# Kernel tuning notes

Hardware: AMD Instinct MI355X
Metric: run time of the kernel (lower is better)

The kernel has to match this reference:

```python
import jax, jax.numpy as jnp
import numpy as np

N, E, IN_DIM, OUT_DIM, HEADS = 50000, 800000, 128, 64, 2
NEG_SLOPE = 0.2  # DGL GATConv default leaky_relu slope


def setup_inputs() -> dict:
    key = jax.random.key(0)
    ks = jax.random.split(key, 11)
    p = lambda k, shape: jax.random.normal(k, shape, jnp.float32) * 0.05
    return dict(
        feature=jax.random.normal(ks[0], (N, IN_DIM), jnp.float32),
        src=jax.random.randint(ks[1], (E,), 0, N, jnp.int32),
        dst=jax.random.randint(ks[2], (E,), 0, N, jnp.int32),
        W1=p(ks[3], (IN_DIM, HEADS * OUT_DIM)),
        al1=p(ks[4], (HEADS, OUT_DIM)),
        ar1=p(ks[5], (HEADS, OUT_DIM)),
        b1=p(ks[6], (HEADS * OUT_DIM,)),
        W2=p(ks[7], (HEADS * OUT_DIM, OUT_DIM)),
        al2=p(ks[8], (1, OUT_DIM)),
        ar2=p(ks[9], (1, OUT_DIM)),
        b2=p(ks[10], (OUT_DIM,)),
    )


def gat_conv(x, W, al, ar, b, src, dst, n_nodes):
    # DGL GATConv (eval mode): fc -> per-node attn halves -> edge leaky_relu
    # -> edge-softmax grouped by dst -> scatter-weighted sum -> + bias
    H, D = al.shape
    h = (x @ W).reshape(n_nodes, H, D)               # [N,H,D]
    el = jnp.einsum('nhd,hd->nh', h, al)             # [N,H]
    er = jnp.einsum('nhd,hd->nh', h, ar)             # [N,H]
    e = jax.nn.leaky_relu(el[src] + er[dst], NEG_SLOPE)  # [E,H]
    m = jax.ops.segment_max(e, dst, num_segments=n_nodes)
    m = jnp.where(jnp.isfinite(m), m, 0.0)           # guard isolated dst nodes
    ex = jnp.exp(e - m[dst])                         # [E,H]
    s = jax.ops.segment_sum(ex, dst, num_segments=n_nodes)
    alpha = ex / s[dst]                              # edge-softmax weights
    out = jax.ops.segment_sum(alpha[:, :, None] * h[src], dst,
                              num_segments=n_nodes)  # [N,H,D]
    return out + b.reshape(H, D)


def reference(feature, src, dst, W1, al1, ar1, b1, W2, al2, ar2, b2):
    h1 = jax.nn.elu(gat_conv(feature, W1, al1, ar1, b1, src, dst, N))  # [N,2,D]
    h2 = gat_conv(h1.reshape(N, -1), W2, al2, ar2, b2, src, dst, N)    # [N,1,D]
    return (h1.mean(axis=1) + h2[:, 0, :]) * 0.5
```

## Files before the change

### kernel.cpp

```cpp
#include <hip/hip_runtime.h>
#include <hip/hip_fp16.h>
#include <math.h>

#define NNODES 50000
#define NEDGES 800000
#define CSR_STRIDE 48
#define NBUCKET 256
#define CHUNK 196
#define BCAP 4096
#define EPB 4096

typedef short bf16x8 __attribute__((ext_vector_type(8)));
typedef float f32x4  __attribute__((ext_vector_type(4)));

__device__ __forceinline__ unsigned bfpack(float a, float b) {
    unsigned ua = __float_as_uint(a), ub = __float_as_uint(b);
    ua = (ua + 0x7fffu + ((ua >> 16) & 1u)) >> 16;
    ub = (ub + 0x7fffu + ((ub >> 16) & 1u)) >> 16;
    return ua | (ub << 16);
}
__device__ __forceinline__ unsigned h2pack(float a, float b) {
    __half2 h = __floats2half2_rn(a, b);
    return *(unsigned*)&h;
}
__device__ __forceinline__ float hlo(unsigned u) {
    union { unsigned u; __half2 h; } c; c.u = u; return __half2float(c.h.x);
}
__device__ __forceinline__ float hhi(unsigned u) {
    union { unsigned u; __half2 h; } c; c.u = u; return __half2float(c.h.y);
}

__global__ __launch_bounds__(256) void bucketA_kernel(
    const int* __restrict__ src, const int* __restrict__ dst,
    int* __restrict__ bcnt, unsigned* __restrict__ bbuf) {
    __shared__ int lcnt[NBUCKET];
    __shared__ int lcur[NBUCKET];
    const int tid = threadIdx.x;
    lcnt[tid] = 0;
    __syncthreads();
    const int e0 = blockIdx.x * EPB;
    int e1 = e0 + EPB; if (e1 > NEDGES) e1 = NEDGES;
    for (int e = e0 + tid; e < e1; e += 256)
        atomicAdd(&lcnt[dst[e] / CHUNK], 1);
    __syncthreads();
    int c = lcnt[tid];
    int base = 0;
    if (c > 0) base = atomicAdd(&bcnt[tid], c);
    lcur[tid] = tid * BCAP + base;
    __syncthreads();
    for (int e = e0 + tid; e < e1; e += 256) {
        int d = dst[e], s = src[e];
        int b = d / CHUNK;
        int pos = atomicAdd(&lcur[b], 1);
        if (pos < (b + 1) * BCAP)
            bbuf[pos] = ((unsigned)(d - b * CHUNK) << 16) | (unsigned)s;
    }
}

__global__ __launch_bounds__(256) void bucketB_kernel(
    const int* __restrict__ bcnt, const unsigned* __restrict__ bbuf,
    int* __restrict__ deg, unsigned short* __restrict__ pcsr) {
    const int b = blockIdx.x, tid = threadIdx.x;
    const int n0 = b * CHUNK;
    int ncnt = NNODES - n0; if (ncnt > CHUNK) ncnt = CHUNK;
    __shared__ int ldeg[CHUNK];
    __shared__ unsigned short lcsr[CHUNK * CSR_STRIDE];
    for (int i = tid; i < CHUNK; i += 256) ldeg[i] = 0;
    __syncthreads();
    int cnt = bcnt[b]; if (cnt > BCAP) cnt = BCAP;
    const unsigned* bb = bbuf + (size_t)b * BCAP;
    for (int i = tid; i < cnt; i += 256) {
        unsigned e = bb[i];
        int ln = e >> 16;
        int p = atomicAdd(&ldeg[ln], 1);
        if (p < CSR_STRIDE) lcsr[ln * CSR_STRIDE + p] = (unsigned short)(e & 0xffffu);
    }
    __syncthreads();
    for (int i = tid; i < ncnt; i += 256) deg[n0 + i] = ldeg[i];
    const int nv = ncnt * (CSR_STRIDE / 8);
    uint4* d4 = (uint4*)(pcsr + (size_t)n0 * CSR_STRIDE);
    const uint4* s4 = (const uint4*)lcsr;
    for (int i = tid; i < nv; i += 256) d4[i] = s4[i];
}

__global__ __launch_bounds__(256) void wt_kernel(const float* __restrict__ W1,
                                                 const float* __restrict__ W2,
                                                 unsigned* __restrict__ W1t,
                                                 unsigned* __restrict__ W2t,
                                                 int* __restrict__ bcnt) {
    if (blockIdx.x == 0) bcnt[threadIdx.x] = 0;
    int w = blockIdx.x * 256 + threadIdx.x;
    if (w < 8192) {
        int n = w >> 6, j = w & 63;
        W1t[w] = bfpack(W1[(2 * j) * 128 + n], W1[(2 * j + 1) * 128 + n]);
    } else {
        int w2 = w - 8192;
        int n = w2 >> 6, j = w2 & 63;
        W2t[w2] = bfpack(W2[(2 * j) * 64 + n], W2[(2 * j + 1) * 64 + n]);
    }
}

__global__ __launch_bounds__(256) void gemm1_kernel(
    const float* __restrict__ feat, const unsigned* __restrict__ Wt,
    const float* __restrict__ al, const float* __restrict__ ar,
    unsigned* __restrict__ h, float* __restrict__ el, float* __restrict__ er) {
    __shared__ unsigned Wb[128 * 68];
    __shared__ unsigned Ab[64 * 68];
    const int tid = threadIdx.x;
    const int n0  = blockIdx.x * 64;

#pragma unroll
    for (int i = 0; i < 8; ++i) {
        int id = i * 256 + tid;
        int n = id >> 4, c = (id & 15) * 4;
        *(uint4*)&Wb[n * 68 + c] = *(const uint4*)&Wt[n * 64 + c];
    }
#pragma unroll
    for (int i = 0; i < 8; ++i) {
        int f = i * 256 + tid;
        int m = f >> 5, cf = (f & 31) * 4;
        float4 v = make_float4(0.f, 0.f, 0.f, 0.f);
        if (n0 + m < NNODES)
            v = *(const float4*)&feat[(size_t)(n0 + m) * 128 + cf];
        uint2 p = {bfpack(v.x, v.y), bfpack(v.z, v.w)};
        *(uint2*)&Ab[m * 68 + cf / 2] = p;
    }
    __syncthreads();

    const int w  = tid >> 6;
    const int l  = tid & 63;
    const int ml = l & 15;
    const int q  = l >> 4;
    f32x4 acc[8];
#pragma unroll
    for (int t = 0; t < 8; ++t) acc[t] = (f32x4){0.f, 0.f, 0.f, 0.f};

#pragma unroll
    for (int kc = 0; kc < 4; ++kc) {
        const int kw = kc * 16 + q * 4;
        uint4 a4 = *(uint4*)&Ab[(16 * w + ml) * 68 + kw];
        bf16x8 af = *(bf16x8*)&a4;
#pragma unroll
        for (int t = 0; t < 8; ++t) {
            uint4 b4 = *(uint4*)&Wb[(t * 16 + ml) * 68 + kw];
            bf16x8 bf = *(bf16x8*)&b4;
            acc[t] = __builtin_amdgcn_mfma_f32_16x16x32_bf16(af, bf, acc[t], 0, 0, 0);
        }
    }

    float av[8], rv[8];
#pragma unroll
    for (int t = 0; t < 8; ++t) { av[t] = al[t * 16 + ml]; rv[t] = ar[t * 16 + ml]; }

#pragma unroll
    for (int r = 0; r < 4; ++r) {
        const int node = n0 + 16 * w + q * 4 + r;
        float e0 = 0.f, e1 = 0.f, f0 = 0.f, f1 = 0.f;
#pragma unroll
        for (int t = 0; t < 8; ++t) {
            float v = acc[t][r];
            if (t < 4) { e0 = fmaf(v, av[t], e0); f0 = fmaf(v, rv[t], f0); }
            else       { e1 = fmaf(v, av[t], e1); f1 = fmaf(v, rv[t], f1); }
            float pv = __shfl_xor(v, 1);
            if ((ml & 1) == 0 && node < NNODES)
                h[(size_t)node * 64 + t * 8 + (ml >> 1)] = h2pack(v, pv);
        }
#pragma unroll
        for (int mm = 1; mm <= 8; mm <<= 1) {
            e0 += __shfl_xor(e0, mm); e1 += __shfl_xor(e1, mm);
            f0 += __shfl_xor(f0, mm); f1 += __shfl_xor(f1, mm);
        }
        if (ml == 0 && node < NNODES) {
            el[node * 2 + 0] = e0; el[node * 2 + 1] = e1;
            er[node * 2 + 0] = f0; er[node * 2 + 1] = f1;
        }
    }
}

__global__ __launch_bounds__(256) void gemm2_kernel(
    const unsigned* __restrict__ h1b, const unsigned* __restrict__ Wt,
    const float* __restrict__ al, const float* __restrict__ ar,
    unsigned* __restrict__ h2, float* __restrict__ el, float* __restrict__ er) {
    __shared__ unsigned Wb[64 * 68];
    __shared__ unsigned Ab[64 * 68];
    const int tid = threadIdx.x;
    const int n0  = blockIdx.x * 64;

#pragma unroll
    for (int i = 0; i < 4; ++i) {
        int id = i * 256 + tid;
        int n = id >> 4, c = (id & 15) * 4;
        *(uint4*)&Wb[n * 68 + c] = *(const uint4*)&Wt[n * 64 + c];
    }
#pragma unroll
    for (int i = 0; i < 4; ++i) {
        int id = i * 256 + tid;
        int m = id >> 4, c = (id & 15) * 4;
        uint4 v = make_uint4(0u, 0u, 0u, 0u);
        if (n0 + m < NNODES)
            v = *(const uint4*)&h1b[(size_t)(n0 + m) * 64 + c];
        *(uint4*)&Ab[m * 68 + c] = v;
    }
    __syncthreads();

    const int w  = tid >> 6;
    const int l  = tid & 63;
    const int ml = l & 15;
    const int q  = l >> 4;
    f32x4 acc[4];
#pragma unroll
    for (int t = 0; t < 4; ++t) acc[t] = (f32x4){0.f, 0.f, 0.f, 0.f};

#pragma unroll
    for (int kc = 0; kc < 4; ++kc) {
        const int kw = kc * 16 + q * 4;
        uint4 a4 = *(uint4*)&Ab[(16 * w + ml) * 68 + kw];
        bf16x8 af = *(bf16x8*)&a4;
#pragma unroll
        for (int t = 0; t < 4; ++t) {
            uint4 b4 = *(uint4*)&Wb[(t * 16 + ml) * 68 + kw];
            bf16x8 bf = *(bf16x8*)&b4;
            acc[t] = __builtin_amdgcn_mfma_f32_16x16x32_bf16(af, bf, acc[t], 0, 0, 0);
        }
    }

    float av[4], rv[4];
#pragma unroll
    for (int t = 0; t < 4; ++t) { av[t] = al[t * 16 + ml]; rv[t] = ar[t * 16 + ml]; }

#pragma unroll
    for (int r = 0; r < 4; ++r) {
        const int node = n0 + 16 * w + q * 4 + r;
        float e0 = 0.f, f0 = 0.f;
#pragma unroll
        for (int t = 0; t < 4; ++t) {
            float v = acc[t][r];
            e0 = fmaf(v, av[t], e0);
            f0 = fmaf(v, rv[t], f0);
            float pv = __shfl_xor(v, 1);
            if ((ml & 1) == 0 && node < NNODES)
                h2[(size_t)node * 32 + t * 8 + (ml >> 1)] = h2pack(v, pv);
        }
#pragma unroll
        for (int mm = 1; mm <= 8; mm <<= 1) {
            e0 += __shfl_xor(e0, mm);
            f0 += __shfl_xor(f0, mm);
        }
        if (ml == 0 && node < NNODES) { el[node] = e0; er[node] = f0; }
    }
}

#define FMA8(hv, A)                                              \
    a0r = fmaf(hlo(hv.x), A, a0r); a1r = fmaf(hhi(hv.x), A, a1r); \
    a2r = fmaf(hlo(hv.y), A, a2r); a3r = fmaf(hhi(hv.y), A, a3r); \
    a4r = fmaf(hlo(hv.z), A, a4r); a5r = fmaf(hhi(hv.z), A, a5r); \
    a6r = fmaf(hlo(hv.w), A, a6r); a7r = fmaf(hhi(hv.w), A, a7r);

__global__ __launch_bounds__(256) void aggregate1_kernel(
    const int* __restrict__ degv,
    const unsigned short* __restrict__ csr_src,
    const float* __restrict__ el, const float* __restrict__ er,
    const unsigned* __restrict__ hh, const float* __restrict__ bias,
    unsigned* __restrict__ h1b, float* __restrict__ hm) {
    const int wid  = (blockIdx.x * 256 + threadIdx.x) >> 6;
    const int lane = threadIdx.x & 63;
    const int g    = lane >> 4;
    const int l16  = lane & 15;
    const int gb   = g * 16;
    const int node = wid * 4 + g;
    if (node >= NNODES) return;
    const int row = node * CSR_STRIDE;
    int deg = degv[node];
    deg = deg < CSR_STRIDE ? deg : CSR_STRIDE;
    const float er0 = er[node * 2 + 0];
    const float er1 = er[node * 2 + 1];
    const bool hsel = (l16 >= 8);
    const unsigned* __restrict__ hq = hh + 4 * l16;

    int s0 = 0;
    if (l16 < deg) s0 = (int)csr_src[row + l16];

    uint4 hv[16];
#pragma unroll
    for (int j = 0; j < 16; ++j) {
        int s = __shfl(s0, gb + j);
        hv[j] = *(const uint4*)(hq + (size_t)s * 64);
    }

    float2 e2 = *(const float2*)&el[s0 * 2];
    float a = e2.x + er0; a = a > 0.f ? a : 0.2f * a;
    float b = e2.y + er1; b = b > 0.f ? b : 0.2f * b;
    float v0 = (l16 < deg) ? a : -1e30f;
    float v1 = (l16 < deg) ? b : -1e30f;
    float m0 = v0, m1 = v1;
    int   s1 = 0, s2 = 0;
    float va1 = -1e30f, vb1 = -1e30f, va2 = -1e30f, vb2 = -1e30f;
    if (deg > 16) {
        if (16 + l16 < deg) {
            s1 = (int)csr_src[row + 16 + l16];
            float2 ee = *(const float2*)&el[s1 * 2];
            float aa = ee.x + er0; va1 = aa > 0.f ? aa : 0.2f * aa;
            float bb = ee.y + er1; vb1 = bb > 0.f ? bb : 0.2f * bb;
            m0 = fmaxf(m0, va1); m1 = fmaxf(m1, vb1);
        }
        if (32 + l16 < deg) {
            s2 = (int)csr_src[row + 32 + l16];
            float2 ee = *(const float2*)&el[s2 * 2];
            float aa = ee.x + er0; va2 = aa > 0.f ? aa : 0.2f * aa;
            float bb = ee.y + er1; vb2 = bb > 0.f ? bb : 0.2f * bb;
            m0 = fmaxf(m0, va2); m1 = fmaxf(m1, vb2);
        }
    }
#pragma unroll
    for (int off = 8; off > 0; off >>= 1) {
        m0 = fmaxf(m0, __shfl_xor(m0, off));
        m1 = fmaxf(m1, __shfl_xor(m1, off));
    }
    float p0 = __expf(v0 - m0),  p1 = __expf(v1 - m1);
    float q0 = __expf(va1 - m0), q1 = __expf(vb1 - m1);
    float r0 = __expf(va2 - m0), r1 = __expf(vb2 - m1);
    float ssum0 = p0 + q0 + r0, ssum1 = p1 + q1 + r1;
#pragma unroll
    for (int off = 8; off > 0; off >>= 1) {
        ssum0 += __shfl_xor(ssum0, off);
        ssum1 += __shfl_xor(ssum1, off);
    }

    float a0r = 0.f, a1r = 0.f, a2r = 0.f, a3r = 0.f;
    float a4r = 0.f, a5r = 0.f, a6r = 0.f, a7r = 0.f;
#pragma unroll
    for (int j = 0; j < 16; ++j) {
        float x = __shfl(p0, gb + j);
        float y = __shfl(p1, gb + j);
        float A = hsel ? y : x;
        FMA8(hv[j], A)
    }
    if (deg > 16) {
        uint4 hw[16];
#pragma unroll
        for (int j = 0; j < 16; ++j) {
            int s = __shfl(s1, gb + j);
            hw[j] = *(const uint4*)(hq + (size_t)s * 64);
        }
#pragma unroll
        for (int j = 0; j < 16; ++j) {
            float x = __shfl(q0, gb + j);
            float y = __shfl(q1, gb + j);
            float A = hsel ? y : x;
            FMA8(hw[j], A)
        }
    }
    if (deg > 32) {
        uint4 hz[16];
#pragma unroll
        for (int j = 0; j < 16; ++j) {
            int s = __shfl(s2, gb + j);
            hz[j] = *(const uint4*)(hq + (size_t)s * 64);
        }
#pragma unroll
        for (int j = 0; j < 16; ++j) {
            float x = __shfl(r0, gb + j);
            float y = __shfl(r1, gb + j);
            float A = hsel ? y : x;
            FMA8(hz[j], A)
        }
    }

    const float ssum = hsel ? ssum1 : ssum0;
    const float inv  = (deg > 0) ? 1.f / ssum : 0.f;
    float4 b0 = *(const float4*)&bias[8 * l16];
    float4 b1 = *(const float4*)&bias[8 * l16 + 4];
    float o0 = fmaf(a0r, inv, b0.x), o1 = fmaf(a1r, inv, b0.y);
    float o2 = fmaf(a2r, inv, b0.z), o3 = fmaf(a3r, inv, b0.w);
    float o4 = fmaf(a4r, inv, b1.x), o5 = fmaf(a5r, inv, b1.y);
    float o6 = fmaf(a6r, inv, b1.z), o7 = fmaf(a7r, inv, b1.w);
    o0 = o0 > 0.f ? o0 : (__expf(o0) - 1.f);
    o1 = o1 > 0.f ? o1 : (__expf(o1) - 1.f);
    o2 = o2 > 0.f ? o2 : (__expf(o2) - 1.f);
    o3 = o3 > 0.f ? o3 : (__expf(o3) - 1.f);
    o4 = o4 > 0.f ? o4 : (__expf(o4) - 1.f);
    o5 = o5 > 0.f ? o5 : (__expf(o5) - 1.f);
    o6 = o6 > 0.f ? o6 : (__expf(o6) - 1.f);
    o7 = o7 > 0.f ? o7 : (__expf(o7) - 1.f);

    uint4 pk;
    pk.x = bfpack(o0, o1); pk.y = bfpack(o2, o3);
    pk.z = bfpack(o4, o5); pk.w = bfpack(o6, o7);
    *(uint4*)&h1b[(size_t)node * 64 + 4 * l16] = pk;

    float n0_ = 0.5f * (o0 + __shfl_xor(o0, 8));
    float n1_ = 0.5f * (o1 + __shfl_xor(o1, 8));
    float n2_ = 0.5f * (o2 + __shfl_xor(o2, 8));
    float n3_ = 0.5f * (o3 + __shfl_xor(o3, 8));
    float n4_ = 0.5f * (o4 + __shfl_xor(o4, 8));
    float n5_ = 0.5f * (o5 + __shfl_xor(o5, 8));
    float n6_ = 0.5f * (o6 + __shfl_xor(o6, 8));
    float n7_ = 0.5f * (o7 + __shfl_xor(o7, 8));
    if (l16 < 8) {
        *(float4*)&hm[(size_t)node * 64 + 8 * l16]     = make_float4(n0_, n1_, n2_, n3_);
        *(float4*)&hm[(size_t)node * 64 + 8 * l16 + 4] = make_float4(n4_, n5_, n6_, n7_);
    }
}

#define FMA4(hv, P)                                            \
    ax = fmaf(hlo(hv.x), P, ax); ay = fmaf(hhi(hv.x), P, ay);  \
    az = fmaf(hlo(hv.y), P, az); aw = fmaf(hhi(hv.y), P, aw);

__global__ __launch_bounds__(256) void aggregate2_kernel(
    const int* __restrict__ degv,
    const unsigned short* __restrict__ csr_src,
    const float* __restrict__ el, const float* __restrict__ er,
    const unsigned* __restrict__ hh, const float* __restrict__ bias,
    const float* __restrict__ hm, float* __restrict__ outp) {
    const int wid  = (blockIdx.x * 256 + threadIdx.x) >> 6;
    const int lane = threadIdx.x & 63;
    const int g    = lane >> 4;
    const int l16  = lane & 15;
    const int gb   = g * 16;
    const int node = wid * 4 + g;
    if (node >= NNODES) return;
    const int row = node * CSR_STRIDE;
    int deg = degv[node];
    deg = deg < CSR_STRIDE ? deg : CSR_STRIDE;
    const float erd = er[node];
    const unsigned* __restrict__ hq = hh + 2 * l16;

    int s0 = 0;
    if (l16 < deg) s0 = (int)csr_src[row + l16];

    uint2 hv[16];
#pragma unroll
    for (int j = 0; j < 16; ++j) {
        int s = __shfl(s0, gb + j);
        hv[j] = *(const uint2*)(hq + (size_t)s * 32);
    }

    float v = el[s0] + erd;
    v = v > 0.f ? v : 0.2f * v;
    float v0 = (l16 < deg) ? v : -1e30f;
    float m = v0;
    int   s1 = 0, s2 = 0;
    float va1 = -1e30f, va2 = -1e30f;
    if (deg > 16) {
        if (16 + l16 < deg) {
            s1 = (int)csr_src[row + 16 + l16];
            float vv = el[s1] + erd;
            va1 = vv > 0.f ? vv : 0.2f * vv;
            m = fmaxf(m, va1);
        }
        if (32 + l16 < deg) {
            s2 = (int)csr_src[row + 32 + l16];
            float vv = el[s2] + erd;
            va2 = vv > 0.f ? vv : 0.2f * vv;
            m = fmaxf(m, va2);
        }
    }
#pragma unroll
    for (int off = 8; off > 0; off >>= 1) m = fmaxf(m, __shfl_xor(m, off));
    float p0 = __expf(v0 - m);
    float q0 = __expf(va1 - m);
    float r0 = __expf(va2 - m);
    float ssum = p0 + q0 + r0;
#pragma unroll
    for (int off = 8; off > 0; off >>= 1) ssum += __shfl_xor(ssum, off);

    float ax = 0.f, ay = 0.f, az = 0.f, aw = 0.f;
#pragma unroll
    for (int j = 0; j < 16; ++j) {
        float p = __shfl(p0, gb + j);
        FMA4(hv[j], p)
    }
    if (deg > 16) {
        uint2 hw[16];
#pragma unroll
        for (int j = 0; j < 16; ++j) {
            int s = __shfl(s1, gb + j);
            hw[j] = *(const uint2*)(hq + (size_t)s * 32);
        }
#pragma unroll
        for (int j = 0; j < 16; ++j) {
            float p = __shfl(q0, gb + j);
            FMA4(hw[j], p)
        }
    }
    if (deg > 32) {
        uint2 hz[16];
#pragma unroll
        for (int j = 0; j < 16; ++j) {
            int s = __shfl(s2, gb + j);
            hz[j] = *(const uint2*)(hq + (size_t)s * 32);
        }
#pragma unroll
        for (int j = 0; j < 16; ++j) {
            float p = __shfl(r0, gb + j);
            FMA4(hz[j], p)
        }
    }

    float inv = (deg > 0) ? 1.f / ssum : 0.f;
    float4 hmv = *(const float4*)&hm[(size_t)node * 64 + 4 * l16];
    float4 bb  = *(const float4*)&bias[4 * l16];
    float o0 = (hmv.x + fmaf(ax, inv, bb.x)) * 0.5f;
    float o1 = (hmv.y + fmaf(ay, inv, bb.y)) * 0.5f;
    float o2 = (hmv.z + fmaf(az, inv, bb.z)) * 0.5f;
    float o3 = (hmv.w + fmaf(aw, inv, bb.w)) * 0.5f;
    *(float4*)&outp[(size_t)node * 64 + 4 * l16] = make_float4(o0, o1, o2, o3);
}


extern "C" void kernel_launch(void* const* d_in, const int* in_sizes, int n_in,
                              void* d_out, int out_size, void* d_ws, size_t ws_size,
                              hipStream_t stream) {
    const float* feat = (const float*)d_in[0];
    const int*   src  = (const int*)d_in[1];
    const int*   dst  = (const int*)d_in[2];
    const float* W1   = (const float*)d_in[3];
    const float* al1  = (const float*)d_in[4];
    const float* ar1  = (const float*)d_in[5];
    const float* b1   = (const float*)d_in[6];
    const float* W2   = (const float*)d_in[7];
    const float* al2  = (const float*)d_in[8];
    const float* ar2  = (const float*)d_in[9];
    const float* b2   = (const float*)d_in[10];
    float* out = (float*)d_out;

    int*            bcnt   = (int*)d_ws;
    int*            ideg   = bcnt + NBUCKET;
    unsigned*       iw1t   = (unsigned*)(ideg + NNODES);
    unsigned*       iw2t   = iw1t + 8192;
    unsigned short* pcsr   = (unsigned short*)(iw2t + 4096);
    unsigned*       gH1    = (unsigned*)(pcsr + (size_t)NNODES * CSR_STRIDE);
    unsigned*       bbuf   = gH1;
    unsigned*       gH2    = gH1;
    unsigned*       h1b    = gH1 + (size_t)NNODES * 64;
    float*          hmean  = (float*)(h1b + (size_t)NNODES * 64);
    float*          fEl1   = hmean + (size_t)NNODES * 64;
    float*          fEr1   = fEl1 + (size_t)NNODES * 2;
    float*          fEl2   = fEr1 + (size_t)NNODES * 2;
    float*          fEr2   = fEl2 + (size_t)NNODES;

    wt_kernel<<<48, 256, 0, stream>>>(W1, W2, iw1t, iw2t, bcnt);
    bucketA_kernel<<<(NEDGES + EPB - 1) / EPB, 256, 0, stream>>>(src, dst, bcnt, bbuf);
    bucketB_kernel<<<NBUCKET, 256, 0, stream>>>(bcnt, bbuf, ideg, pcsr);

    gemm1_kernel<<<(NNODES + 63) / 64, 256, 0, stream>>>(feat, iw1t, al1, ar1,
                                                         gH1, fEl1, fEr1);
    aggregate1_kernel<<<(NNODES + 15) / 16, 256, 0, stream>>>(
        ideg, pcsr, fEl1, fEr1, gH1, b1, h1b, hmean);

    gemm2_kernel<<<(NNODES + 63) / 64, 256, 0, stream>>>(h1b, iw2t, al2, ar2,
                                                         gH2, fEl2, fEr2);
    aggregate2_kernel<<<(NNODES + 15) / 16, 256, 0, stream>>>(
        ideg, pcsr, fEl2, fEr2, gH2, b2, hmean, out);
}
```

Baseline: 207.9 us.

## Merge independent prep stages into shared launches to cut kernel count

Folds weight transposition into the edge-bucketing kernel as extra blocks, and runs CSR build blocks inside the gemm1 launch since the two are independent. The bucket counter is now zeroed with a memset. The bucket buffer moves to the h1b region so it no longer aliases gH1, which gemm1 writes while CSR build blocks are still reading buckets. This removes launch gaps and lets independent work overlap, at the cost of branchy kernels with shared LDS sizing.

```diff
diff --git a/kernel.cpp b/kernel.cpp
--- a/kernel.cpp
+++ b/kernel.cpp
@@ -9,6 +9,8 @@
 #define CHUNK 196
 #define BCAP 4096
 #define EPB 4096
+#define NBLK_A ((NEDGES + EPB - 1) / EPB)
+#define NBLK_G1 ((NNODES + 63) / 64)
 
 typedef short bf16x8 __attribute__((ext_vector_type(8)));
 typedef float f32x4  __attribute__((ext_vector_type(4)));
@@ -30,84 +32,84 @@
     union { unsigned u; __half2 h; } c; c.u = u; return __half2float(c.h.y);
 }
 
-__global__ __launch_bounds__(256) void bucketA_kernel(
+__global__ __launch_bounds__(256) void prep_kernel(
     const int* __restrict__ src, const int* __restrict__ dst,
-    int* __restrict__ bcnt, unsigned* __restrict__ bbuf) {
-    __shared__ int lcnt[NBUCKET];
-    __shared__ int lcur[NBUCKET];
+    int* __restrict__ bcnt, unsigned* __restrict__ bbuf,
+    const float* __restrict__ W1, const float* __restrict__ W2,
+    unsigned* __restrict__ W1t, unsigned* __restrict__ W2t) {
     const int tid = threadIdx.x;
-    lcnt[tid] = 0;
-    __syncthreads();
-    const int e0 = blockIdx.x * EPB;
-    int e1 = e0 + EPB; if (e1 > NEDGES) e1 = NEDGES;
-    for (int e = e0 + tid; e < e1; e += 256)
-        atomicAdd(&lcnt[dst[e] / CHUNK], 1);
-    __syncthreads();
-    int c = lcnt[tid];
-    int base = 0;
-    if (c > 0) base = atomicAdd(&bcnt[tid], c);
-    lcur[tid] = tid * BCAP + base;
-    __syncthreads();
-    for (int e = e0 + tid; e < e1; e += 256) {
-        int d = dst[e], s = src[e];
-        int b = d / CHUNK;
-        int pos = atomicAdd(&lcur[b], 1);
-        if (pos < (b + 1) * BCAP)
-            bbuf[pos] = ((unsigned)(d - b * CHUNK) << 16) | (unsigned)s;
-    }
-}
-
-__global__ __launch_bounds__(256) void bucketB_kernel(
+    if (blockIdx.x < NBLK_A) {
+        __shared__ int lcnt[NBUCKET];
+        __shared__ int lcur[NBUCKET];
+        lcnt[tid] = 0;
+        __syncthreads();
+        const int e0 = blockIdx.x * EPB;
+        int e1 = e0 + EPB; if (e1 > NEDGES) e1 = NEDGES;
+        for (int e = e0 + tid; e < e1; e += 256)
+            atomicAdd(&lcnt[dst[e] / CHUNK], 1);
+        __syncthreads();
+        int c = lcnt[tid];
+        int base = 0;
+        if (c > 0) base = atomicAdd(&bcnt[tid], c);
+        lcur[tid] = tid * BCAP + base;
+        __syncthreads();
+        for (int e = e0 + tid; e < e1; e += 256) {
+            int d = dst[e], s = src[e];
+            int b = d / CHUNK;
+            int pos = atomicAdd(&lcur[b], 1);
+            if (pos < (b + 1) * BCAP)
+                bbuf[pos] = ((unsigned)(d - b * CHUNK) << 16) | (unsigned)s;
+        }
+    } else {
+        int w = (blockIdx.x - NBLK_A) * 256 + tid;
+        if (w < 8192) {
+            int n = w >> 6, j = w & 63;
+            W1t[w] = bfpack(W1[(2 * j) * 128 + n], W1[(2 * j + 1) * 128 + n]);
+        } else {
+            int w2 = w - 8192;
+            int n = w2 >> 6, j = w2 & 63;
+            W2t[w2] = bfpack(W2[(2 * j) * 64 + n], W2[(2 * j + 1) * 64 + n]);
+        }
+    }
+}
+
+__global__ __launch_bounds__(256) void build_gemm1_kernel(
     const int* __restrict__ bcnt, const unsigned* __restrict__ bbuf,
-    int* __restrict__ deg, unsigned short* __restrict__ pcsr) {
-    const int b = blockIdx.x, tid = threadIdx.x;
-    const int n0 = b * CHUNK;
-    int ncnt = NNODES - n0; if (ncnt > CHUNK) ncnt = CHUNK;
-    __shared__ int ldeg[CHUNK];
-    __shared__ unsigned short lcsr[CHUNK * CSR_STRIDE];
-    for (int i = tid; i < CHUNK; i += 256) ldeg[i] = 0;
-    __syncthreads();
-    int cnt = bcnt[b]; if (cnt > BCAP) cnt = BCAP;
-    const unsigned* bb = bbuf + (size_t)b * BCAP;
-    for (int i = tid; i < cnt; i += 256) {
-        unsigned e = bb[i];
-        int ln = e >> 16;
-        int p = atomicAdd(&ldeg[ln], 1);
-        if (p < CSR_STRIDE) lcsr[ln * CSR_STRIDE + p] = (unsigned short)(e & 0xffffu);
-    }
-    __syncthreads();
-    for (int i = tid; i < ncnt; i += 256) deg[n0 + i] = ldeg[i];
-    const int nv = ncnt * (CSR_STRIDE / 8);
-    uint4* d4 = (uint4*)(pcsr + (size_t)n0 * CSR_STRIDE);
-    const uint4* s4 = (const uint4*)lcsr;
-    for (int i = tid; i < nv; i += 256) d4[i] = s4[i];
-}
-
-__global__ __launch_bounds__(256) void wt_kernel(const float* __restrict__ W1,
-                                                 const float* __restrict__ W2,
-                                                 unsigned* __restrict__ W1t,
-                                                 unsigned* __restrict__ W2t,
-                                                 int* __restrict__ bcnt) {
-    if (blockIdx.x == 0) bcnt[threadIdx.x] = 0;
-    int w = blockIdx.x * 256 + threadIdx.x;
-    if (w < 8192) {
-        int n = w >> 6, j = w & 63;
-        W1t[w] = bfpack(W1[(2 * j) * 128 + n], W1[(2 * j + 1) * 128 + n]);
-    } else {
-        int w2 = w - 8192;
-        int n = w2 >> 6, j = w2 & 63;
-        W2t[w2] = bfpack(W2[(2 * j) * 64 + n], W2[(2 * j + 1) * 64 + n]);
-    }
-}
-
-__global__ __launch_bounds__(256) void gemm1_kernel(
+    int* __restrict__ deg, unsigned short* __restrict__ pcsr,
     const float* __restrict__ feat, const unsigned* __restrict__ Wt,
     const float* __restrict__ al, const float* __restrict__ ar,
     unsigned* __restrict__ h, float* __restrict__ el, float* __restrict__ er) {
-    __shared__ unsigned Wb[128 * 68];
-    __shared__ unsigned Ab[64 * 68];
+    __shared__ uint4 smem4[(128 * 68 + 64 * 68) / 4];
     const int tid = threadIdx.x;
-    const int n0  = blockIdx.x * 64;
+
+    if (blockIdx.x < NBUCKET) {
+        int* ldeg = (int*)smem4;
+        unsigned short* lcsr = (unsigned short*)(ldeg + CHUNK);
+        const int b = blockIdx.x;
+        const int n0 = b * CHUNK;
+        int ncnt = NNODES - n0; if (ncnt > CHUNK) ncnt = CHUNK;
+        for (int i = tid; i < CHUNK; i += 256) ldeg[i] = 0;
+        __syncthreads();
+        int cnt = bcnt[b]; if (cnt > BCAP) cnt = BCAP;
+        const unsigned* bb = bbuf + (size_t)b * BCAP;
+        for (int i = tid; i < cnt; i += 256) {
+            unsigned e = bb[i];
+            int ln = e >> 16;
+            int p = atomicAdd(&ldeg[ln], 1);
+            if (p < CSR_STRIDE) lcsr[ln * CSR_STRIDE + p] = (unsigned short)(e & 0xffffu);
+        }
+        __syncthreads();
+        for (int i = tid; i < ncnt; i += 256) deg[n0 + i] = ldeg[i];
+        const int nv = ncnt * (CSR_STRIDE / 8);
+        uint4* d4 = (uint4*)(pcsr + (size_t)n0 * CSR_STRIDE);
+        const uint4* s4 = (const uint4*)lcsr;
+        for (int i = tid; i < nv; i += 256) d4[i] = s4[i];
+        return;
+    }
+
+    unsigned* Wb = (unsigned*)smem4;
+    unsigned* Ab = Wb + 128 * 68;
+    const int n0 = (blockIdx.x - NBUCKET) * 64;
 
 #pragma unroll
     for (int i = 0; i < 8; ++i) {
@@ -530,26 +532,24 @@
     unsigned*       iw2t   = iw1t + 8192;
     unsigned short* pcsr   = (unsigned short*)(iw2t + 4096);
     unsigned*       gH1    = (unsigned*)(pcsr + (size_t)NNODES * CSR_STRIDE);
-    unsigned*       bbuf   = gH1;
     unsigned*       gH2    = gH1;
     unsigned*       h1b    = gH1 + (size_t)NNODES * 64;
+    unsigned*       bbuf   = h1b;
     float*          hmean  = (float*)(h1b + (size_t)NNODES * 64);
     float*          fEl1   = hmean + (size_t)NNODES * 64;
     float*          fEr1   = fEl1 + (size_t)NNODES * 2;
     float*          fEl2   = fEr1 + (size_t)NNODES * 2;
     float*          fEr2   = fEl2 + (size_t)NNODES;
 
-    wt_kernel<<<48, 256, 0, stream>>>(W1, W2, iw1t, iw2t, bcnt);
-    bucketA_kernel<<<(NEDGES + EPB - 1) / EPB, 256, 0, stream>>>(src, dst, bcnt, bbuf);
-    bucketB_kernel<<<NBUCKET, 256, 0, stream>>>(bcnt, bbuf, ideg, pcsr);
-
-    gemm1_kernel<<<(NNODES + 63) / 64, 256, 0, stream>>>(feat, iw1t, al1, ar1,
-                                                         gH1, fEl1, fEr1);
+    hipMemsetAsync(bcnt, 0, NBUCKET * sizeof(int), stream);
+    prep_kernel<<<NBLK_A + 48, 256, 0, stream>>>(src, dst, bcnt, bbuf,
+                                                 W1, W2, iw1t, iw2t);
+    build_gemm1_kernel<<<NBUCKET + NBLK_G1, 256, 0, stream>>>(
+        bcnt, bbuf, ideg, pcsr, feat, iw1t, al1, ar1, gH1, fEl1, fEr1);
     aggregate1_kernel<<<(NNODES + 15) / 16, 256, 0, stream>>>(
         ideg, pcsr, fEl1, fEr1, gH1, b1, h1b, hmean);
-
-    gemm2_kernel<<<(NNODES + 63) / 64, 256, 0, stream>>>(h1b, iw2t, al2, ar2,
-                                                         gH2, fEl2, fEr2);
+    gemm2_kernel<<<NBLK_G1, 256, 0, stream>>>(h1b, iw2t, al2, ar2,
+                                              gH2, fEl2, fEr2);
     aggregate2_kernel<<<(NNODES + 15) / 16, 256, 0, stream>>>(
         ideg, pcsr, fEl2, fEr2, gH2, b2, hmean, out);
 }
```

New measurement: 199.8 us, median of 2. 1.04x faster.
